# Kernel optimization log

Measured on AMD Instinct MI355X. Metric: run time of the kernel, lower is better.

Reference implementation:

```python
import jax, jax.numpy as jnp
import numpy as np

L, V, C, H, T_MAX, FF = 8, 50257, 1024, 16, 1024, 4096
DH = C // H
EPS = 1e-5


def setup_inputs() -> dict:
    key = jax.random.key(0)
    ks = jax.random.split(key, 16)
    s = 0.02
    inp = {
        "idx": jax.random.randint(ks[0], (2, 1024), 0, V, dtype=jnp.int32),
        "tok_emb": jax.random.normal(ks[1], (V, C), jnp.float32) * s,
        "pos_emb": jax.random.normal(ks[2], (T_MAX, C), jnp.float32) * s,
        "qkv_w": jax.random.normal(ks[3], (L, C, 3 * C), jnp.float32) * s,
        "qkv_b": jnp.zeros((L, 3 * C), jnp.float32),
        "out_w": jax.random.normal(ks[4], (L, C, C), jnp.float32) * s,
        "out_b": jnp.zeros((L, C), jnp.float32),
        "ln1_s": jnp.ones((L, C), jnp.float32),
        "ln1_b": jnp.zeros((L, C), jnp.float32),
        "ln2_s": jnp.ones((L, C), jnp.float32),
        "ln2_b": jnp.zeros((L, C), jnp.float32),
        "ffn_w1": jax.random.normal(ks[5], (L, C, FF), jnp.float32) * s,
        "ffn_b1": jnp.zeros((L, FF), jnp.float32),
        "ffn_w2": jax.random.normal(ks[6], (L, FF, C), jnp.float32) * s,
        "ffn_b2": jnp.zeros((L, C), jnp.float32),
        "lnf_s": jnp.ones((C,), jnp.float32),
        "lnf_b": jnp.zeros((C,), jnp.float32),
    }
    return inp


def _layernorm(x, scale, bias):
    m = jnp.mean(x, axis=-1, keepdims=True)
    v = jnp.mean(jnp.square(x - m), axis=-1, keepdims=True)
    return (x - m) * jax.lax.rsqrt(v + EPS) * scale + bias


def reference(idx, tok_emb, pos_emb, qkv_w, qkv_b, out_w, out_b,
              ln1_s, ln1_b, ln2_s, ln2_b,
              ffn_w1, ffn_b1, ffn_w2, ffn_b2, lnf_s, lnf_b):
    B, T = idx.shape
    x = tok_emb[idx] + pos_emb[:T]          # [B,T,C]
    causal = jnp.tril(jnp.ones((T, T), bool))  # [T,T]
    scale = 1.0 / np.sqrt(DH)

    def block(x, p):
        qw, qb, ow, ob, l1s, l1b, l2s, l2b, w1, b1, w2, b2 = p
        h = _layernorm(x, l1s, l1b)
        qkv = h @ qw + qb                    # [B,T,3C]
        q, k, v = jnp.split(qkv, 3, axis=-1)
        q = q.reshape(B, T, H, DH).transpose(0, 2, 1, 3)  # [B,H,T,Dh]
        k = k.reshape(B, T, H, DH).transpose(0, 2, 1, 3)
        v = v.reshape(B, T, H, DH).transpose(0, 2, 1, 3)
        scores = jnp.einsum('bhqd,bhkd->bhqk', q, k) * scale
        scores = jnp.where(causal, scores, -jnp.inf)
        w = jax.nn.softmax(scores, axis=-1)
        o = jnp.einsum('bhqk,bhkd->bhqd', w, v)
        o = o.transpose(0, 2, 1, 3).reshape(B, T, C)
        x = x + (o @ ow + ob)
        h2 = _layernorm(x, l2s, l2b)
        x = x + (jax.nn.gelu(h2 @ w1 + b1, approximate=False) @ w2 + b2)
        return x, None

    params = (qkv_w, qkv_b, out_w, out_b, ln1_s, ln1_b, ln2_s, ln2_b,
              ffn_w1, ffn_b1, ffn_w2, ffn_b2)
    x, _ = jax.lax.scan(block, x, params)
    x = _layernorm(x, lnf_s, lnf_b)
    logits = x @ tok_emb.T                   # tied head, no bias
    return logits
```

## Files before the change

kernel.cpp:

```cpp
#include <hip/hip_runtime.h>
#include <hip/hip_bf16.h>

#define NL 8
#define NV 50257
#define NC 1024
#define NH 16
#define NT 1024
#define NFF 4096
#define NB 2
#define NM (NB*NT)

typedef __attribute__((ext_vector_type(8))) short bf16x8;
typedef __attribute__((ext_vector_type(4))) float f32x4;

__device__ __forceinline__ unsigned short f2bf(float f) {
    union { float f; unsigned u; } a; a.f = f;
    unsigned r = a.u + 0x7FFFu + ((a.u >> 16) & 1u);
    return (unsigned short)(r >> 16);
}

__device__ __forceinline__ void gload16(const unsigned short* g, unsigned short* l) {
    __builtin_amdgcn_global_load_lds(
        (const __attribute__((address_space(1))) unsigned int*)g,
        (__attribute__((address_space(3))) unsigned int*)l,
        16, 0, 0);
}

template<int VN> __device__ __forceinline__ void vwait() {
    asm volatile("s_waitcnt vmcnt(%0)" :: "n"(VN) : "memory");
}
__device__ __forceinline__ void barrier_mem() {
    asm volatile("" ::: "memory");
    __builtin_amdgcn_s_barrier();
    asm volatile("" ::: "memory");
}

__global__ __launch_bounds__(256) void embed_kernel(
    const int* __restrict__ idx, const float* __restrict__ te,
    const float* __restrict__ pe, float* __restrict__ x) {
    int row = blockIdx.x;
    int t = row & (NT - 1);
    int id = idx[row];
    const float4 a = reinterpret_cast<const float4*>(te + (size_t)id * NC)[threadIdx.x];
    const float4 b = reinterpret_cast<const float4*>(pe + (size_t)t * NC)[threadIdx.x];
    float4 o; o.x = a.x + b.x; o.y = a.y + b.y; o.z = a.z + b.z; o.w = a.w + b.w;
    reinterpret_cast<float4*>(x + (size_t)row * NC)[threadIdx.x] = o;
}

__global__ __launch_bounds__(256) void cvt_bf16_kernel(
    const float* __restrict__ in, unsigned short* __restrict__ out, size_t n4) {
    size_t i = (size_t)blockIdx.x * 256 + threadIdx.x;
    if (i >= n4) return;
    float4 v = reinterpret_cast<const float4*>(in)[i];
    uint2 u;
    u.x = (unsigned)f2bf(v.x) | ((unsigned)f2bf(v.y) << 16);
    u.y = (unsigned)f2bf(v.z) | ((unsigned)f2bf(v.w) << 16);
    reinterpret_cast<uint2*>(out)[i] = u;
}

__global__ __launch_bounds__(256) void wtrans_kernel(
    const float* __restrict__ W, unsigned short* __restrict__ Wt, int K, int N) {
    __shared__ float tile[32][33];
    int n0 = blockIdx.x * 32, k0 = blockIdx.y * 32;
    int tx = threadIdx.x, ty = threadIdx.y;
#pragma unroll
    for (int i = 0; i < 4; ++i)
        tile[ty + i * 8][tx] = W[(size_t)(k0 + ty + i * 8) * N + n0 + tx];
    __syncthreads();
#pragma unroll
    for (int i = 0; i < 4; ++i)
        Wt[(size_t)(n0 + ty + i * 8) * K + k0 + tx] = f2bf(tile[tx][ty + i * 8]);
}

__global__ __launch_bounds__(256) void ln_kernel(
    const float* __restrict__ x, const float* __restrict__ gam,
    const float* __restrict__ bet, unsigned short* __restrict__ out) {
    __shared__ float red[4];
    int row = blockIdx.x, tid = threadIdx.x;
    const float4 v = reinterpret_cast<const float4*>(x + (size_t)row * NC)[tid];
    float s = v.x + v.y + v.z + v.w;
#pragma unroll
    for (int m = 32; m >= 1; m >>= 1) s += __shfl_xor(s, m, 64);
    if ((tid & 63) == 0) red[tid >> 6] = s;
    __syncthreads();
    float mean = (red[0] + red[1] + red[2] + red[3]) * (1.0f / NC);
    __syncthreads();
    float dx = v.x - mean, dy = v.y - mean, dz = v.z - mean, dw = v.w - mean;
    float q = dx * dx + dy * dy + dz * dz + dw * dw;
#pragma unroll
    for (int m = 32; m >= 1; m >>= 1) q += __shfl_xor(q, m, 64);
    if ((tid & 63) == 0) red[tid >> 6] = q;
    __syncthreads();
    float var = (red[0] + red[1] + red[2] + red[3]) * (1.0f / NC);
    float rstd = rsqrtf(var + 1e-5f);
    int c = tid * 4;
    const float4 g4 = reinterpret_cast<const float4*>(gam)[tid];
    const float4 b4 = reinterpret_cast<const float4*>(bet)[tid];
    uint2 u;
    u.x = (unsigned)f2bf(dx * rstd * g4.x + b4.x) |
          ((unsigned)f2bf(dy * rstd * g4.y + b4.y) << 16);
    u.y = (unsigned)f2bf(dz * rstd * g4.z + b4.z) |
          ((unsigned)f2bf(dw * rstd * g4.w + b4.w) << 16);
    reinterpret_cast<uint2*>(out + (size_t)row * NC + c)[0] = u;
}

template<int ACT, bool BIAS, bool OUTBF16, bool NEDGE, bool ATOMIC>
__global__ __launch_bounds__(256) void gemm_kernel(
    const unsigned short* __restrict__ A, const unsigned short* __restrict__ Bt,
    const float* __restrict__ bias, void* __restrict__ Cout,
    int N, int K, int ldc, int ksub) {
    __shared__ unsigned short As[128 * 32];
    __shared__ unsigned short Bs[128 * 32];
    const int tid = threadIdx.x;
    const int lane = tid & 63;
    const int wave = tid >> 6;
    const int wm = wave >> 1, wn = wave & 1;
    const int lr = lane & 15, lg = lane >> 4;
    const int m0 = blockIdx.x * 128, n0 = blockIdx.y * 128;
    const int kbeg = blockIdx.z * ksub, kend = kbeg + ksub;

    const int r0 = tid >> 2;
    const int c0 = (tid & 3) * 8;
    int bn0 = n0 + r0, bn1 = n0 + r0 + 64;
    if (NEDGE) { bn0 = min(bn0, N - 1); bn1 = min(bn1, N - 1); }
    const unsigned short* Ag0 = A + (size_t)(m0 + r0) * K + c0;
    const unsigned short* Ag1 = A + (size_t)(m0 + r0 + 64) * K + c0;
    const unsigned short* Bg0 = Bt + (size_t)bn0 * K + c0;
    const unsigned short* Bg1 = Bt + (size_t)bn1 * K + c0;
    unsigned short* Al0 = As + wave * 512;
    unsigned short* Al1 = As + 2048 + wave * 512;
    unsigned short* Bl0 = Bs + wave * 512;
    unsigned short* Bl1 = Bs + 2048 + wave * 512;

    const f32x4 zero4 = {0.0f, 0.0f, 0.0f, 0.0f};
    f32x4 acc[4][4];
#pragma unroll
    for (int i = 0; i < 4; ++i)
#pragma unroll
        for (int j = 0; j < 4; ++j) acc[i][j] = zero4;

    for (int k0 = kbeg; k0 < kend; k0 += 32) {
        __syncthreads();
        gload16(Ag0 + k0, Al0);
        gload16(Ag1 + k0, Al1);
        gload16(Bg0 + k0, Bl0);
        gload16(Bg1 + k0, Bl1);
        __syncthreads();
        bf16x8 af[4], bfr[4];
#pragma unroll
        for (int f = 0; f < 4; ++f) {
            af[f]  = *reinterpret_cast<const bf16x8*>(As + (wm * 64 + f * 16 + lr) * 32 + lg * 8);
            bfr[f] = *reinterpret_cast<const bf16x8*>(Bs + (wn * 64 + f * 16 + lr) * 32 + lg * 8);
        }
#pragma unroll
        for (int i = 0; i < 4; ++i)
#pragma unroll
            for (int j = 0; j < 4; ++j)
                acc[i][j] = __builtin_amdgcn_mfma_f32_16x16x32_bf16(af[i], bfr[j], acc[i][j], 0, 0, 0);
    }

#pragma unroll
    for (int i = 0; i < 4; ++i) {
#pragma unroll
        for (int j = 0; j < 4; ++j) {
            int col = n0 + wn * 64 + j * 16 + lr;
            if (NEDGE && col >= N) continue;
            float bv = (BIAS && kbeg == 0) ? bias[col] : 0.0f;
#pragma unroll
            for (int r = 0; r < 4; ++r) {
                int row = m0 + wm * 64 + i * 16 + lg * 4 + r;
                float v = acc[i][j][r] + bv;
                if (ACT == 1) v = 0.5f * v * (1.0f + erff(v * 0.70710678118654752f));
                if (ATOMIC) {
                    atomicAdd(reinterpret_cast<float*>(Cout) + (size_t)row * ldc + col, v);
                } else if (OUTBF16) {
                    reinterpret_cast<unsigned short*>(Cout)[(size_t)row * ldc + col] = f2bf(v);
                } else {
                    reinterpret_cast<float*>(Cout)[(size_t)row * ldc + col] = v;
                }
            }
        }
    }
}

__global__ __launch_bounds__(512, 2) void head_gemm_kernel(
    const unsigned short* __restrict__ A, const unsigned short* __restrict__ Bt,
    float* __restrict__ C, int N, int K) {
    __shared__ unsigned short lds[4][2][8192];
    const int tid = threadIdx.x;
    const int lane = tid & 63, wid = tid >> 6;
    const int wm = wid >> 2, wn = wid & 3;
    const int lr = lane & 15, lg = lane >> 4;

    const int qx = gridDim.x >> 3;
    const int orig = blockIdx.x;
    const int wg = (orig & 7) * qx + (orig >> 3);
    const int m0 = (wg & 7) * 256;
    const int n0 = (wg >> 3) * 256;

    const int o0 = tid, o1 = tid + 512;
    int rA0, kb0, rA1, kb1;
    { int pr = o0 >> 3, s = o0 & 7; int li = (s << 4) ^ ((pr & 7) << 4);
      rA0 = (pr << 1) | (li >> 6); kb0 = li & 63; }
    { int pr = o1 >> 3, s = o1 & 7; int li = (s << 4) ^ ((pr & 7) << 4);
      rA1 = (pr << 1) | (li >> 6); kb1 = li & 63; }
    const char* pA0 = (const char*)A + (size_t)(m0 + rA0) * (2 * K) + kb0;
    const char* pA1 = (const char*)A + (size_t)(m0 + rA1) * (2 * K) + kb1;
    const char* pB0 = (const char*)Bt + (size_t)min(n0 + rA0, N - 1) * (2 * K) + kb0;
    const char* pB1 = (const char*)Bt + (size_t)min(n0 + rA1, N - 1) * (2 * K) + kb1;
    const int dw0 = wid * 512;
    const int dw1 = 4096 + wid * 512;

    const int swz = (((lr & 1) << 6) | (lg << 4)) ^ (((lr >> 1) & 7) << 4);
    const int pbA = (wm * 64 + (lr >> 1)) * 128 + swz;
    const int pbB = (wn * 32 + (lr >> 1)) * 128 + swz;

    auto stage = [&](int slot, int koff) {
        unsigned short* la = &lds[slot][0][0];
        unsigned short* lb = &lds[slot][1][0];
        gload16((const unsigned short*)(pA0 + koff), la + dw0);
        gload16((const unsigned short*)(pA1 + koff), la + dw1);
        gload16((const unsigned short*)(pB0 + koff), lb + dw0);
        gload16((const unsigned short*)(pB1 + koff), lb + dw1);
    };
    auto rdA = [&](int slot, int mf) -> bf16x8 {
        return *reinterpret_cast<const bf16x8*>(
            (const char*)lds + slot * 32768 + pbA + mf * 1024);
    };
    auto rdB = [&](int slot, int nf) -> bf16x8 {
        return *reinterpret_cast<const bf16x8*>(
            (const char*)lds + slot * 32768 + 16384 + pbB + nf * 1024);
    };

    const f32x4 zero4 = {0.0f, 0.0f, 0.0f, 0.0f};
    f32x4 acc[8][4];
#pragma unroll
    for (int i = 0; i < 8; ++i)
#pragma unroll
        for (int j = 0; j < 4; ++j) acc[i][j] = zero4;

#define MFMA_ROW(AF, MI) \
    acc[MI][0] = __builtin_amdgcn_mfma_f32_16x16x32_bf16(AF, bf0, acc[MI][0], 0, 0, 0); \
    acc[MI][1] = __builtin_amdgcn_mfma_f32_16x16x32_bf16(AF, bf1, acc[MI][1], 0, 0, 0); \
    acc[MI][2] = __builtin_amdgcn_mfma_f32_16x16x32_bf16(AF, bf2, acc[MI][2], 0, 0, 0); \
    acc[MI][3] = __builtin_amdgcn_mfma_f32_16x16x32_bf16(AF, bf3, acc[MI][3], 0, 0, 0);

    stage(0, 0);
    stage(1, 64);
    const int nk = K >> 6;
    for (int t = 0; t < nk; ++t) {
        const int cur = (t & 1) << 1;
        const int koff = t << 7;
        const bool pf = (t + 1 < nk);
        vwait<4>();
        barrier_mem();
        if (pf) stage(cur ^ 2, koff + 128);
        bf16x8 bf0 = rdB(cur, 0), bf1 = rdB(cur, 1), bf2 = rdB(cur, 2), bf3 = rdB(cur, 3);
        bf16x8 a0 = rdA(cur, 0), a1 = rdA(cur, 1), a2 = rdA(cur, 2), a3 = rdA(cur, 3);
        __builtin_amdgcn_s_setprio(1);
        MFMA_ROW(a0, 0) MFMA_ROW(a1, 1) MFMA_ROW(a2, 2) MFMA_ROW(a3, 3)
        __builtin_amdgcn_s_setprio(0);
        if (pf) stage((cur ^ 2) | 1, koff + 192);
        a0 = rdA(cur, 4); a1 = rdA(cur, 5); a2 = rdA(cur, 6); a3 = rdA(cur, 7);
        __builtin_amdgcn_s_setprio(1);
        MFMA_ROW(a0, 4) MFMA_ROW(a1, 5) MFMA_ROW(a2, 6) MFMA_ROW(a3, 7)
        __builtin_amdgcn_s_setprio(0);
        if (pf) vwait<8>(); else vwait<0>();
        barrier_mem();
        const int nxt = cur | 1;
        bf0 = rdB(nxt, 0); bf1 = rdB(nxt, 1); bf2 = rdB(nxt, 2); bf3 = rdB(nxt, 3);
        a0 = rdA(nxt, 0); a1 = rdA(nxt, 1); a2 = rdA(nxt, 2); a3 = rdA(nxt, 3);
        __builtin_amdgcn_s_setprio(1);
        MFMA_ROW(a0, 0) MFMA_ROW(a1, 1) MFMA_ROW(a2, 2) MFMA_ROW(a3, 3)
        __builtin_amdgcn_s_setprio(0);
        a0 = rdA(nxt, 4); a1 = rdA(nxt, 5); a2 = rdA(nxt, 6); a3 = rdA(nxt, 7);
        __builtin_amdgcn_s_setprio(1);
        MFMA_ROW(a0, 4) MFMA_ROW(a1, 5) MFMA_ROW(a2, 6) MFMA_ROW(a3, 7)
        __builtin_amdgcn_s_setprio(0);
    }
#undef MFMA_ROW

#pragma unroll
    for (int mf = 0; mf < 8; ++mf)
#pragma unroll
        for (int nf = 0; nf < 4; ++nf) {
            int col = n0 + wn * 64 + nf * 16 + lr;
            if (col < N) {
#pragma unroll
                for (int r = 0; r < 4; ++r) {
                    int row = m0 + wm * 128 + mf * 16 + lg * 4 + r;
                    C[(size_t)row * N + col] = acc[mf][nf][r];
                }
            }
        }
}

__global__ __launch_bounds__(256) void vtrans_kernel(
    const unsigned short* __restrict__ qkv, unsigned short* __restrict__ vt) {
    __shared__ unsigned short tile[32][33];
    int bh = blockIdx.z; int b = bh >> 4, h = bh & 15;
    int t0 = blockIdx.x * 32, d0 = blockIdx.y * 32;
    int tx = threadIdx.x, ty = threadIdx.y;
#pragma unroll
    for (int i = 0; i < 4; ++i)
        tile[ty + i * 8][tx] =
            qkv[(size_t)(b * NT + t0 + ty + i * 8) * 3072 + 2048 + h * 64 + d0 + tx];
    __syncthreads();
#pragma unroll
    for (int i = 0; i < 4; ++i)
        vt[((size_t)(b * NH + h) * 64 + d0 + ty + i * 8) * NT + t0 + tx] = tile[tx][ty + i * 8];
}

__global__ __launch_bounds__(64) void attn_kernel(
    const unsigned short* __restrict__ qkv, const unsigned short* __restrict__ vt,
    unsigned short* __restrict__ o) {
    __shared__ unsigned short Vs[64][72];
    __shared__ unsigned short Ps[32][72];
    const int qt = blockIdx.x;
    const int h  = blockIdx.y;
    const int b  = blockIdx.z;
    const int lane = threadIdx.x;
    const int lr = lane & 15, lg = lane >> 4;

    const unsigned short* qbase = qkv + (size_t)(b * NT + qt * 32) * 3072 + h * 64;
    bf16x8 qf[2][2];
#pragma unroll
    for (int mf = 0; mf < 2; ++mf)
#pragma unroll
        for (int kc = 0; kc < 2; ++kc)
            qf[mf][kc] = *reinterpret_cast<const bf16x8*>(
                qbase + (size_t)(mf * 16 + lr) * 3072 + kc * 32 + lg * 8);

    const f32x4 zero4 = {0.0f, 0.0f, 0.0f, 0.0f};
    f32x4 oacc[2][4];
    float mrow[2][4], lsum[2][4];
#pragma unroll
    for (int mf = 0; mf < 2; ++mf) {
#pragma unroll
        for (int nf = 0; nf < 4; ++nf) oacc[mf][nf] = zero4;
#pragma unroll
        for (int r = 0; r < 4; ++r) { mrow[mf][r] = -INFINITY; lsum[mf][r] = 0.0f; }
    }

    const int qend = qt * 32 + 32;
    const int nkt = (qend + 63) >> 6;
    const unsigned short* kbase = qkv + (size_t)(b * NT) * 3072 + NC + h * 64;
    const unsigned short* vbase = vt + (size_t)((b * NH + h) * 64) * NT;

    for (int kt = 0; kt < nkt; ++kt) {
        __syncthreads();
#pragma unroll
        for (int i = 0; i < 8; ++i) {
            int chunk = lane + i * 64;
            int d = chunk >> 3;
            int kk = (chunk & 7) * 8;
            *reinterpret_cast<bf16x8*>(&Vs[d][kk]) =
                *reinterpret_cast<const bf16x8*>(vbase + (size_t)d * NT + kt * 64 + kk);
        }
        f32x4 s[2][4];
#pragma unroll
        for (int mf = 0; mf < 2; ++mf)
#pragma unroll
            for (int jf = 0; jf < 4; ++jf) s[mf][jf] = zero4;
#pragma unroll
        for (int kc = 0; kc < 2; ++kc) {
            bf16x8 kf[4];
#pragma unroll
            for (int jf = 0; jf < 4; ++jf)
                kf[jf] = *reinterpret_cast<const bf16x8*>(
                    kbase + (size_t)(kt * 64 + jf * 16 + lr) * 3072 + kc * 32 + lg * 8);
#pragma unroll
            for (int mf = 0; mf < 2; ++mf)
#pragma unroll
                for (int jf = 0; jf < 4; ++jf)
                    s[mf][jf] = __builtin_amdgcn_mfma_f32_16x16x32_bf16(
                        qf[mf][kc], kf[jf], s[mf][jf], 0, 0, 0);
        }
        const bool lastt = (kt == nkt - 1);
#pragma unroll
        for (int mf = 0; mf < 2; ++mf) {
#pragma unroll
            for (int r = 0; r < 4; ++r) {
                int rowg = qt * 32 + mf * 16 + lg * 4 + r;
                float tmax = -INFINITY;
#pragma unroll
                for (int jf = 0; jf < 4; ++jf) {
                    float v = s[mf][jf][r] * 0.125f;
                    if (lastt) {
                        int colg = kt * 64 + jf * 16 + lr;
                        if (colg > rowg) v = -INFINITY;
                    }
                    s[mf][jf][r] = v;
                    tmax = fmaxf(tmax, v);
                }
                tmax = fmaxf(tmax, __shfl_xor(tmax, 1, 64));
                tmax = fmaxf(tmax, __shfl_xor(tmax, 2, 64));
                tmax = fmaxf(tmax, __shfl_xor(tmax, 4, 64));
                tmax = fmaxf(tmax, __shfl_xor(tmax, 8, 64));
                float mnew = fmaxf(mrow[mf][r], tmax);
                float corr = __expf(mrow[mf][r] - mnew);
                float ps = 0.0f;
#pragma unroll
                for (int jf = 0; jf < 4; ++jf) {
                    float p = __expf(s[mf][jf][r] - mnew);
                    s[mf][jf][r] = p;
                    ps += p;
                }
                ps += __shfl_xor(ps, 1, 64);
                ps += __shfl_xor(ps, 2, 64);
                ps += __shfl_xor(ps, 4, 64);
                ps += __shfl_xor(ps, 8, 64);
                lsum[mf][r] = lsum[mf][r] * corr + ps;
                mrow[mf][r] = mnew;
#pragma unroll
                for (int nf = 0; nf < 4; ++nf) oacc[mf][nf][r] *= corr;
            }
        }
#pragma unroll
        for (int mf = 0; mf < 2; ++mf)
#pragma unroll
            for (int jf = 0; jf < 4; ++jf)
#pragma unroll
                for (int r = 0; r < 4; ++r)
                    Ps[mf * 16 + lg * 4 + r][jf * 16 + lr] = f2bf(s[mf][jf][r]);
        __syncthreads();
#pragma unroll
        for (int kc = 0; kc < 2; ++kc) {
            bf16x8 pf[2], vf[4];
#pragma unroll
            for (int mf = 0; mf < 2; ++mf)
                pf[mf] = *reinterpret_cast<const bf16x8*>(&Ps[mf * 16 + lr][kc * 32 + lg * 8]);
#pragma unroll
            for (int nf = 0; nf < 4; ++nf)
                vf[nf] = *reinterpret_cast<const bf16x8*>(&Vs[nf * 16 + lr][kc * 32 + lg * 8]);
#pragma unroll
            for (int mf = 0; mf < 2; ++mf)
#pragma unroll
                for (int nf = 0; nf < 4; ++nf)
                    oacc[mf][nf] = __builtin_amdgcn_mfma_f32_16x16x32_bf16(
                        pf[mf], vf[nf], oacc[mf][nf], 0, 0, 0);
        }
    }

    unsigned short* ob = o + (size_t)(b * NT + qt * 32) * NC + h * 64;
#pragma unroll
    for (int mf = 0; mf < 2; ++mf)
#pragma unroll
        for (int nf = 0; nf < 4; ++nf)
#pragma unroll
            for (int r = 0; r < 4; ++r) {
                float v = oacc[mf][nf][r] / lsum[mf][r];
                ob[(size_t)(mf * 16 + lg * 4 + r) * NC + nf * 16 + lr] = f2bf(v);
            }
}

extern "C" void kernel_launch(void* const* d_in, const int* in_sizes, int n_in,
                              void* d_out, int out_size, void* d_ws, size_t ws_size,
                              hipStream_t stream) {
    (void)in_sizes; (void)n_in; (void)out_size; (void)ws_size;
    const int*   idx    = (const int*)  d_in[0];
    const float* tok    = (const float*)d_in[1];
    const float* pos    = (const float*)d_in[2];
    const float* qkv_w  = (const float*)d_in[3];
    const float* qkv_b  = (const float*)d_in[4];
    const float* out_w  = (const float*)d_in[5];
    const float* out_b  = (const float*)d_in[6];
    const float* ln1_s  = (const float*)d_in[7];
    const float* ln1_b  = (const float*)d_in[8];
    const float* ln2_s  = (const float*)d_in[9];
    const float* ln2_b  = (const float*)d_in[10];
    const float* ffn_w1 = (const float*)d_in[11];
    const float* ffn_b1 = (const float*)d_in[12];
    const float* ffn_w2 = (const float*)d_in[13];
    const float* ffn_b2 = (const float*)d_in[14];
    const float* lnf_s  = (const float*)d_in[15];
    const float* lnf_b  = (const float*)d_in[16];

    char* p = (char*)d_ws;
    float* x              = (float*)p;          p += (size_t)NM * NC * 4;
    unsigned short* hbuf  = (unsigned short*)p; p += (size_t)NM * NC * 2;
    unsigned short* qkvb  = (unsigned short*)p; p += (size_t)NM * 3 * NC * 2;
    unsigned short* obuf  = (unsigned short*)p; p += (size_t)NM * NC * 2;
    unsigned short* gbuf  = (unsigned short*)p; p += (size_t)NM * NFF * 2;
    unsigned short* vtb   = (unsigned short*)p; p += (size_t)NB * NH * 64 * NT * 2;
    unsigned short* wq    = (unsigned short*)p; p += (size_t)3 * NC * NC * 2;
    unsigned short* wo    = (unsigned short*)p; p += (size_t)NC * NC * 2;
    unsigned short* w1    = (unsigned short*)p; p += (size_t)NC * NFF * 2;
    unsigned short* w2    = (unsigned short*)p; p += (size_t)NFF * NC * 2;
    unsigned short* temb  = (unsigned short*)p; p += (size_t)NV * NC * 2;

    {
        size_t n4 = (size_t)NV * NC / 4;
        int blocks = (int)((n4 + 255) / 256);
        cvt_bf16_kernel<<<blocks, 256, 0, stream>>>(tok, temb, n4);
    }
    embed_kernel<<<NM, 256, 0, stream>>>(idx, tok, pos, x);

    for (int l = 0; l < NL; ++l) {
        wtrans_kernel<<<dim3(96, 32),  dim3(32, 8), 0, stream>>>(qkv_w + (size_t)l * NC * 3 * NC, wq, NC, 3 * NC);
        wtrans_kernel<<<dim3(32, 32),  dim3(32, 8), 0, stream>>>(out_w + (size_t)l * NC * NC, wo, NC, NC);
        wtrans_kernel<<<dim3(128, 32), dim3(32, 8), 0, stream>>>(ffn_w1 + (size_t)l * NC * NFF, w1, NC, NFF);
        wtrans_kernel<<<dim3(32, 128), dim3(32, 8), 0, stream>>>(ffn_w2 + (size_t)l * NFF * NC, w2, NFF, NC);

        ln_kernel<<<NM, 256, 0, stream>>>(x, ln1_s + (size_t)l * NC, ln1_b + (size_t)l * NC, hbuf);
        gemm_kernel<0, true, true, false, false><<<dim3(16, 24), 256, 0, stream>>>(
            hbuf, wq, qkv_b + (size_t)l * 3 * NC, qkvb, 3 * NC, NC, 3 * NC, NC);
        vtrans_kernel<<<dim3(32, 2, 32), dim3(32, 8), 0, stream>>>(qkvb, vtb);
        attn_kernel<<<dim3(32, 16, 2), 64, 0, stream>>>(qkvb, vtb, obuf);
        gemm_kernel<0, true, false, false, true><<<dim3(16, 8, 2), 256, 0, stream>>>(
            obuf, wo, out_b + (size_t)l * NC, x, NC, NC, NC, NC / 2);
        ln_kernel<<<NM, 256, 0, stream>>>(x, ln2_s + (size_t)l * NC, ln2_b + (size_t)l * NC, hbuf);
        gemm_kernel<1, true, true, false, false><<<dim3(16, 32), 256, 0, stream>>>(
            hbuf, w1, ffn_b1 + (size_t)l * NFF, gbuf, NFF, NC, NFF, NC);
        gemm_kernel<0, true, false, false, true><<<dim3(16, 8, 4), 256, 0, stream>>>(
            gbuf, w2, ffn_b2 + (size_t)l * NC, x, NC, NFF, NC, NFF / 4);
    }
    ln_kernel<<<NM, 256, 0, stream>>>(x, lnf_s, lnf_b, hbuf);
    head_gemm_kernel<<<dim3(8 * 197), 512, 0, stream>>>(hbuf, temb, (float*)d_out, NV, NC);
}
```

Measured before the change: 2.220 ms.

## Double-buffer GEMM LDS tiles and merge per-layer weight transposes into one launch

The GEMM kernel now uses two LDS buffers for A and B. It issues the next k-tile's global-to-LDS loads before computing on the current tile, with one barrier per iteration instead of two. The four per-layer weight transpose launches are fused into a single kernel that dispatches on block index. The unused N-edge template path is removed. Double buffering doubles LDS use per block, which may reduce occupancy.

```diff
diff --git a/kernel.cpp b/kernel.cpp
--- a/kernel.cpp
+++ b/kernel.cpp
@@ -58,10 +58,19 @@
     reinterpret_cast<uint2*>(out)[i] = u;
 }
 
-__global__ __launch_bounds__(256) void wtrans_kernel(
-    const float* __restrict__ W, unsigned short* __restrict__ Wt, int K, int N) {
+__global__ __launch_bounds__(256) void wtrans4_kernel(
+    const float* __restrict__ s0, const float* __restrict__ s1,
+    const float* __restrict__ s2, const float* __restrict__ s3,
+    unsigned short* __restrict__ d0, unsigned short* __restrict__ d1,
+    unsigned short* __restrict__ d2, unsigned short* __restrict__ d3) {
     __shared__ float tile[32][33];
-    int n0 = blockIdx.x * 32, k0 = blockIdx.y * 32;
+    int bid = blockIdx.x;
+    const float* W; unsigned short* D; int K, N, tn, tk;
+    if (bid < 3072)      { W = s0; D = d0; K = 1024; N = 3072; tn = bid % 96;  tk = bid / 96; }
+    else if (bid < 4096) { int t = bid - 3072; W = s1; D = d1; K = 1024; N = 1024; tn = t & 31;  tk = t >> 5; }
+    else if (bid < 8192) { int t = bid - 4096; W = s2; D = d2; K = 1024; N = 4096; tn = t & 127; tk = t >> 7; }
+    else                 { int t = bid - 8192; W = s3; D = d3; K = 4096; N = 1024; tn = t & 31;  tk = t >> 5; }
+    int n0 = tn * 32, k0 = tk * 32;
     int tx = threadIdx.x, ty = threadIdx.y;
 #pragma unroll
     for (int i = 0; i < 4; ++i)
@@ -69,7 +78,7 @@
     __syncthreads();
 #pragma unroll
     for (int i = 0; i < 4; ++i)
-        Wt[(size_t)(n0 + ty + i * 8) * K + k0 + tx] = f2bf(tile[tx][ty + i * 8]);
+        D[(size_t)(n0 + ty + i * 8) * K + k0 + tx] = f2bf(tile[tx][ty + i * 8]);
 }
 
 __global__ __launch_bounds__(256) void ln_kernel(
@@ -104,13 +113,13 @@
     reinterpret_cast<uint2*>(out + (size_t)row * NC + c)[0] = u;
 }
 
-template<int ACT, bool BIAS, bool OUTBF16, bool NEDGE, bool ATOMIC>
+template<int ACT, bool BIAS, bool OUTBF16, bool ATOMIC>
 __global__ __launch_bounds__(256) void gemm_kernel(
     const unsigned short* __restrict__ A, const unsigned short* __restrict__ Bt,
     const float* __restrict__ bias, void* __restrict__ Cout,
     int N, int K, int ldc, int ksub) {
-    __shared__ unsigned short As[128 * 32];
-    __shared__ unsigned short Bs[128 * 32];
+    __shared__ unsigned short As[2][128 * 32];
+    __shared__ unsigned short Bs[2][128 * 32];
     const int tid = threadIdx.x;
     const int lane = tid & 63;
     const int wave = tid >> 6;
@@ -121,16 +130,12 @@
 
     const int r0 = tid >> 2;
     const int c0 = (tid & 3) * 8;
-    int bn0 = n0 + r0, bn1 = n0 + r0 + 64;
-    if (NEDGE) { bn0 = min(bn0, N - 1); bn1 = min(bn1, N - 1); }
     const unsigned short* Ag0 = A + (size_t)(m0 + r0) * K + c0;
     const unsigned short* Ag1 = A + (size_t)(m0 + r0 + 64) * K + c0;
-    const unsigned short* Bg0 = Bt + (size_t)bn0 * K + c0;
-    const unsigned short* Bg1 = Bt + (size_t)bn1 * K + c0;
-    unsigned short* Al0 = As + wave * 512;
-    unsigned short* Al1 = As + 2048 + wave * 512;
-    unsigned short* Bl0 = Bs + wave * 512;
-    unsigned short* Bl1 = Bs + 2048 + wave * 512;
+    const unsigned short* Bg0 = Bt + (size_t)(n0 + r0) * K + c0;
+    const unsigned short* Bg1 = Bt + (size_t)(n0 + r0 + 64) * K + c0;
+    const int dw0 = wave * 512;
+    const int dw1 = 2048 + wave * 512;
 
     const f32x4 zero4 = {0.0f, 0.0f, 0.0f, 0.0f};
     f32x4 acc[4][4];
@@ -139,24 +144,31 @@
 #pragma unroll
         for (int j = 0; j < 4; ++j) acc[i][j] = zero4;
 
+    auto stage = [&](int buf, int k0) {
+        gload16(Ag0 + k0, &As[buf][dw0]);
+        gload16(Ag1 + k0, &As[buf][dw1]);
+        gload16(Bg0 + k0, &Bs[buf][dw0]);
+        gload16(Bg1 + k0, &Bs[buf][dw1]);
+    };
+
+    stage(0, kbeg);
+    __syncthreads();
+    int cur = 0;
     for (int k0 = kbeg; k0 < kend; k0 += 32) {
-        __syncthreads();
-        gload16(Ag0 + k0, Al0);
-        gload16(Ag1 + k0, Al1);
-        gload16(Bg0 + k0, Bl0);
-        gload16(Bg1 + k0, Bl1);
-        __syncthreads();
+        if (k0 + 32 < kend) stage(cur ^ 1, k0 + 32);
         bf16x8 af[4], bfr[4];
 #pragma unroll
         for (int f = 0; f < 4; ++f) {
-            af[f]  = *reinterpret_cast<const bf16x8*>(As + (wm * 64 + f * 16 + lr) * 32 + lg * 8);
-            bfr[f] = *reinterpret_cast<const bf16x8*>(Bs + (wn * 64 + f * 16 + lr) * 32 + lg * 8);
+            af[f]  = *reinterpret_cast<const bf16x8*>(&As[cur][(wm * 64 + f * 16 + lr) * 32 + lg * 8]);
+            bfr[f] = *reinterpret_cast<const bf16x8*>(&Bs[cur][(wn * 64 + f * 16 + lr) * 32 + lg * 8]);
         }
 #pragma unroll
         for (int i = 0; i < 4; ++i)
 #pragma unroll
             for (int j = 0; j < 4; ++j)
                 acc[i][j] = __builtin_amdgcn_mfma_f32_16x16x32_bf16(af[i], bfr[j], acc[i][j], 0, 0, 0);
+        __syncthreads();
+        cur ^= 1;
     }
 
 #pragma unroll
@@ -164,7 +176,6 @@
 #pragma unroll
         for (int j = 0; j < 4; ++j) {
             int col = n0 + wn * 64 + j * 16 + lr;
-            if (NEDGE && col >= N) continue;
             float bv = (BIAS && kbeg == 0) ? bias[col] : 0.0f;
 #pragma unroll
             for (int r = 0; r < 4; ++r) {
@@ -497,22 +508,22 @@
     embed_kernel<<<NM, 256, 0, stream>>>(idx, tok, pos, x);
 
     for (int l = 0; l < NL; ++l) {
-        wtrans_kernel<<<dim3(96, 32),  dim3(32, 8), 0, stream>>>(qkv_w + (size_t)l * NC * 3 * NC, wq, NC, 3 * NC);
-        wtrans_kernel<<<dim3(32, 32),  dim3(32, 8), 0, stream>>>(out_w + (size_t)l * NC * NC, wo, NC, NC);
-        wtrans_kernel<<<dim3(128, 32), dim3(32, 8), 0, stream>>>(ffn_w1 + (size_t)l * NC * NFF, w1, NC, NFF);
-        wtrans_kernel<<<dim3(32, 128), dim3(32, 8), 0, stream>>>(ffn_w2 + (size_t)l * NFF * NC, w2, NFF, NC);
+        wtrans4_kernel<<<12288, dim3(32, 8), 0, stream>>>(
+            qkv_w + (size_t)l * NC * 3 * NC, out_w + (size_t)l * NC * NC,
+            ffn_w1 + (size_t)l * NC * NFF, ffn_w2 + (size_t)l * NFF * NC,
+            wq, wo, w1, w2);
 
         ln_kernel<<<NM, 256, 0, stream>>>(x, ln1_s + (size_t)l * NC, ln1_b + (size_t)l * NC, hbuf);
-        gemm_kernel<0, true, true, false, false><<<dim3(16, 24), 256, 0, stream>>>(
+        gemm_kernel<0, true, true, false><<<dim3(16, 24), 256, 0, stream>>>(
             hbuf, wq, qkv_b + (size_t)l * 3 * NC, qkvb, 3 * NC, NC, 3 * NC, NC);
         vtrans_kernel<<<dim3(32, 2, 32), dim3(32, 8), 0, stream>>>(qkvb, vtb);
         attn_kernel<<<dim3(32, 16, 2), 64, 0, stream>>>(qkvb, vtb, obuf);
-        gemm_kernel<0, true, false, false, true><<<dim3(16, 8, 2), 256, 0, stream>>>(
+        gemm_kernel<0, true, false, true><<<dim3(16, 8, 2), 256, 0, stream>>>(
             obuf, wo, out_b + (size_t)l * NC, x, NC, NC, NC, NC / 2);
         ln_kernel<<<NM, 256, 0, stream>>>(x, ln2_s + (size_t)l * NC, ln2_b + (size_t)l * NC, hbuf);
-        gemm_kernel<1, true, true, false, false><<<dim3(16, 32), 256, 0, stream>>>(
+        gemm_kernel<1, true, true, false><<<dim3(16, 32), 256, 0, stream>>>(
             hbuf, w1, ffn_b1 + (size_t)l * NFF, gbuf, NFF, NC, NFF, NC);
-        gemm_kernel<0, true, false, false, true><<<dim3(16, 8, 4), 256, 0, stream>>>(
+        gemm_kernel<0, true, false, true><<<dim3(16, 8, 4), 256, 0, stream>>>(
             gbuf, w2, ffn_b2 + (size_t)l * NC, x, NC, NFF, NC, NFF / 4);
     }
     ln_kernel<<<NM, 256, 0, stream>>>(x, lnf_s, lnf_b, hbuf);
```

Result: faster. 2.012 ms (-9.4%).
